# Kernel tuning notes

Measured on AMD Instinct MI355X. Metric: run time of the kernel, lower is better.

Reference implementation:

```python
import jax, jax.numpy as jnp
import numpy as np

NUM_USERS = 100000
NUM_ITEMS = 50000
N_NODES = NUM_USERS + NUM_ITEMS
D = 64
N_LAYERS = 3
E = 2000000
B = 1024
ALPHA_PREF = 1.0


def setup_inputs() -> dict:
    key = jax.random.key(0)
    k1, k2, k3, k4 = jax.random.split(key, 4)
    embed = jax.random.normal(k1, (N_NODES, D), dtype=jnp.float32) * 0.1
    edge_index = jax.random.randint(k2, (2, E), 0, N_NODES, dtype=jnp.int32)
    users = jax.random.randint(k3, (B,), 0, NUM_USERS, dtype=jnp.int32)
    items = jax.random.randint(k4, (B,), 0, NUM_ITEMS, dtype=jnp.int32)
    return {"embed": embed, "edge_index": edge_index, "users": users, "items": items}


def _lightgcn_propagate(x, row, col, norm):
    # message: norm * x[row] (x_j = source), aggregated (add) at col (target)
    msg = norm[:, None] * x[row]                      # [E, D]
    return jnp.zeros_like(x).at[col].add(msg)         # [N, D]


def reference(embed, edge_index, users, items):
    row, col = edge_index[0], edge_index[1]
    n = embed.shape[0]
    # degree normalization (depends only on edge_index; same every layer)
    deg = jnp.zeros((n,), jnp.float32).at[row].add(1.0)
    deg_inv = jnp.clip(deg, 1.0, None) ** -0.5
    norm = deg_inv[row] * deg_inv[col]                # [E]

    x = embed
    for _ in range(N_LAYERS):
        x = _lightgcn_propagate(x, row, col, norm)

    u_emb = x[users]                                  # [B, D]
    i_emb = x[items + NUM_USERS]                      # [B, D]

    # mask = (row == users[:,None]) flattened selection of col; edge e is
    # selected once per batch element b with users[b] == row[e] -> multiplicity
    cnt = jnp.zeros((n,), jnp.float32).at[users].add(1.0)
    mult = cnt[row]                                   # [E] selection multiplicity

    # PreferenceShapley surrogate: softmax over selected neighbor embeddings
    # of alpha_pref * <neigh_emb, mean(u_emb)>, flattened over the batch.
    context = u_emb.mean(0)                           # [D]
    neigh = x[col]                                    # [E, D]
    logits = ALPHA_PREF * (neigh @ context)           # [E]
    masked = jnp.where(mult > 0, logits, -jnp.inf)
    mx = jnp.max(masked)
    ew = mult * jnp.exp(logits - mx)                  # [E] weighted exp (0 where unselected)
    z = jnp.clip(ew.sum(), 1e-12, None)
    neigh_aggr = (ew[:, None] * neigh).sum(0) / z     # [D]

    score = (u_emb * i_emb).sum(-1) + u_emb @ neigh_aggr  # [B]
    return jax.nn.sigmoid(score)
```

## Files before the change

kernel.cpp:

```cpp
#include <hip/hip_runtime.h>
#include <float.h>
#include <math.h>

#define NUM_USERS 100000
#define NUM_ITEMS 50000
#define NNODES    150000
#define DIM       64
#define NEDGE     2000000
#define BATCH     1024
#define SEL_CAP   (1 << 18)
#define LOGIT_BLOCKS 512

#define SLICES   512
#define EPS      3908
#define NBUK     293

__device__ __forceinline__ float wave_sum64(float v) {
    #pragma unroll
    for (int off = 32; off > 0; off >>= 1) v += __shfl_xor(v, off, 64);
    return v;
}

__device__ __forceinline__ float bf2f(unsigned short s) {
    return __uint_as_float(((unsigned int)s) << 16);
}
__device__ __forceinline__ unsigned short f2bf(float f) {
    unsigned int u = __float_as_uint(f);
    return (unsigned short)((u + 0x7fffu + ((u >> 16) & 1u)) >> 16);
}


__global__ __launch_bounds__(512) void bhist_kernel(
        const int* __restrict__ row, const int* __restrict__ col,
        const int* __restrict__ ucnt,
        unsigned short* __restrict__ cntR, unsigned short* __restrict__ cntC,
        unsigned char* __restrict__ rkR, unsigned char* __restrict__ rkC,
        int* __restrict__ n_sel, int* __restrict__ sel_col, float* __restrict__ sel_w) {
    __shared__ unsigned int hr[NBUK], hc[NBUK];
    __shared__ int lcnt, lbase;
    __shared__ int2 buf[256];
    int blk = blockIdx.x, t = threadIdx.x;
    for (int i = t; i < NBUK; i += 512) { hr[i] = 0; hc[i] = 0; }
    if (t == 0) lcnt = 0;
    __syncthreads();
    int e0 = blk * EPS;
    int e1 = e0 + EPS; if (e1 > NEDGE) e1 = NEDGE;
    for (int base = e0 + t * 4; base < e1; base += 2048) {
        if (base + 4 <= e1) {
            int4 r4 = *(const int4*)(row + base);
            int4 c4 = *(const int4*)(col + base);
            uchar4 a, b;
            a.x = (unsigned char)atomicAdd(&hr[r4.x >> 9], 1u);
            a.y = (unsigned char)atomicAdd(&hr[r4.y >> 9], 1u);
            a.z = (unsigned char)atomicAdd(&hr[r4.z >> 9], 1u);
            a.w = (unsigned char)atomicAdd(&hr[r4.w >> 9], 1u);
            b.x = (unsigned char)atomicAdd(&hc[c4.x >> 9], 1u);
            b.y = (unsigned char)atomicAdd(&hc[c4.y >> 9], 1u);
            b.z = (unsigned char)atomicAdd(&hc[c4.z >> 9], 1u);
            b.w = (unsigned char)atomicAdd(&hc[c4.w >> 9], 1u);
            *(uchar4*)(rkR + base) = a;
            *(uchar4*)(rkC + base) = b;
            int u0 = ucnt[r4.x], u1 = ucnt[r4.y], u2 = ucnt[r4.z], u3 = ucnt[r4.w];
            if (u0 > 0) { int i = atomicAdd(&lcnt, 1); if (i < 256) buf[i] = make_int2(c4.x, u0); }
            if (u1 > 0) { int i = atomicAdd(&lcnt, 1); if (i < 256) buf[i] = make_int2(c4.y, u1); }
            if (u2 > 0) { int i = atomicAdd(&lcnt, 1); if (i < 256) buf[i] = make_int2(c4.z, u2); }
            if (u3 > 0) { int i = atomicAdd(&lcnt, 1); if (i < 256) buf[i] = make_int2(c4.w, u3); }
        } else {
            for (int e = base; e < e1; ++e) {
                int r = row[e], c = col[e];
                rkR[e] = (unsigned char)atomicAdd(&hr[r >> 9], 1u);
                rkC[e] = (unsigned char)atomicAdd(&hc[c >> 9], 1u);
                int u = ucnt[r];
                if (u > 0) { int i = atomicAdd(&lcnt, 1); if (i < 256) buf[i] = make_int2(c, u); }
            }
        }
    }
    __syncthreads();
    for (int i = t; i < NBUK; i += 512) {
        cntR[(size_t)blk * NBUK + i] = (unsigned short)hr[i];
        cntC[(size_t)blk * NBUK + i] = (unsigned short)hc[i];
    }
    if (t == 0) {
        int c = lcnt; c = c < 256 ? c : 256;
        lbase = atomicAdd(n_sel, c);
    }
    __syncthreads();
    int c = lcnt; c = c < 256 ? c : 256;
    int b = lbase;
    for (int i = t; i < c; i += 512) {
        int o = b + i;
        if (o < SEL_CAP) { sel_col[o] = buf[i].x; sel_w[o] = (float)buf[i].y; }
    }
}


__global__ __launch_bounds__(512) void bprefix1_kernel(
        const unsigned short* __restrict__ cntR, const unsigned short* __restrict__ cntC,
        unsigned short* __restrict__ offR, unsigned short* __restrict__ offC,
        int* __restrict__ totRC) {
    int side = blockIdx.x / NBUK;
    int b = blockIdx.x - side * NBUK;
    const unsigned short* cnt = side ? cntC : cntR;
    unsigned short* off = side ? offC : offR;
    __shared__ int sm[512];
    int t = threadIdx.x;
    int v = (int)cnt[(size_t)t * NBUK + b];
    sm[t] = v;
    __syncthreads();
    for (int o = 1; o < 512; o <<= 1) {
        int x = (t >= o) ? sm[t - o] : 0;
        __syncthreads();
        sm[t] += x;
        __syncthreads();
    }
    off[(size_t)t * NBUK + b] = (unsigned short)(sm[t] - v);
    if (t == 511) totRC[side * NBUK + b] = sm[511];
}

__global__ __launch_bounds__(512) void bprefix2_kernel(
        const int* __restrict__ totRC, int* __restrict__ baseR, int* __restrict__ baseC) {
    const int* tot = totRC + blockIdx.x * NBUK;
    int* base = blockIdx.x ? baseC : baseR;
    __shared__ int sm[512];
    int t = threadIdx.x;
    int v = (t < NBUK) ? tot[t] : 0;
    sm[t] = v;
    __syncthreads();
    for (int o = 1; o < 512; o <<= 1) {
        int x = (t >= o) ? sm[t - o] : 0;
        __syncthreads();
        sm[t] += x;
        __syncthreads();
    }
    if (t < NBUK) base[t] = sm[t] - v;
    if (t == NBUK - 1) base[NBUK] = sm[t];
}


__global__ __launch_bounds__(512) void place_kernel(
        const int* __restrict__ row, const int* __restrict__ col,
        const unsigned char* __restrict__ rkR, const unsigned char* __restrict__ rkC,
        const unsigned short* __restrict__ cntR, const unsigned short* __restrict__ cntC,
        const unsigned short* __restrict__ offR, const unsigned short* __restrict__ offC,
        const int* __restrict__ baseR, const int* __restrict__ baseC,
        unsigned short* __restrict__ midR, unsigned int* __restrict__ midC) {
    __shared__ int lofC[NBUK], lofR[NBUK], posC[NBUK], posR[NBUK];
    __shared__ int cCl[NBUK], cRl[NBUK];
    __shared__ int scan_tmp[512];
    __shared__ unsigned int   stC[EPS];
    __shared__ unsigned short stR[EPS];
    int blk = blockIdx.x, t = threadIdx.x;
    if (t < NBUK) {
        cCl[t] = (int)cntC[(size_t)blk * NBUK + t];
        cRl[t] = (int)cntR[(size_t)blk * NBUK + t];
        posC[t] = baseC[t] + (int)offC[(size_t)blk * NBUK + t];
        posR[t] = baseR[t] + (int)offR[(size_t)blk * NBUK + t];
    }
    __syncthreads();
    scan_tmp[t] = (t < NBUK) ? cCl[t] : 0;
    __syncthreads();
    for (int o = 1; o < 512; o <<= 1) {
        int v = (t >= o) ? scan_tmp[t - o] : 0;
        __syncthreads();
        scan_tmp[t] += v;
        __syncthreads();
    }
    if (t < NBUK) lofC[t] = scan_tmp[t] - cCl[t];
    __syncthreads();
    scan_tmp[t] = (t < NBUK) ? cRl[t] : 0;
    __syncthreads();
    for (int o = 1; o < 512; o <<= 1) {
        int v = (t >= o) ? scan_tmp[t - o] : 0;
        __syncthreads();
        scan_tmp[t] += v;
        __syncthreads();
    }
    if (t < NBUK) lofR[t] = scan_tmp[t] - cRl[t];
    __syncthreads();
    int e0 = blk * EPS;
    int e1 = e0 + EPS; if (e1 > NEDGE) e1 = NEDGE;
    for (int base = e0 + t * 4; base < e1; base += 2048) {
        if (base + 4 <= e1) {
            int4 r4 = *(const int4*)(row + base);
            int4 c4 = *(const int4*)(col + base);
            uchar4 kr = *(const uchar4*)(rkR + base);
            uchar4 kc = *(const uchar4*)(rkC + base);
            stC[lofC[c4.x >> 9] + (int)kc.x] = ((unsigned int)(c4.x & 511) << 18) | (unsigned int)r4.x;
            stC[lofC[c4.y >> 9] + (int)kc.y] = ((unsigned int)(c4.y & 511) << 18) | (unsigned int)r4.y;
            stC[lofC[c4.z >> 9] + (int)kc.z] = ((unsigned int)(c4.z & 511) << 18) | (unsigned int)r4.z;
            stC[lofC[c4.w >> 9] + (int)kc.w] = ((unsigned int)(c4.w & 511) << 18) | (unsigned int)r4.w;
            stR[lofR[r4.x >> 9] + (int)kr.x] = (unsigned short)(r4.x & 511);
            stR[lofR[r4.y >> 9] + (int)kr.y] = (unsigned short)(r4.y & 511);
            stR[lofR[r4.z >> 9] + (int)kr.z] = (unsigned short)(r4.z & 511);
            stR[lofR[r4.w >> 9] + (int)kr.w] = (unsigned short)(r4.w & 511);
        } else {
            for (int e = base; e < e1; ++e) {
                int r = row[e], c = col[e];
                stC[lofC[c >> 9] + (int)rkC[e]] = ((unsigned int)(c & 511) << 18) | (unsigned int)r;
                stR[lofR[r >> 9] + (int)rkR[e]] = (unsigned short)(r & 511);
            }
        }
    }
    __syncthreads();
    int wave = t >> 6, lane = t & 63;
    for (int b = wave; b < NBUK; b += 8) {
        int n = cCl[b], lo = lofC[b], dst = posC[b];
        for (int i = lane; i < n; i += 64) midC[dst + i] = stC[lo + i];
        n = cRl[b]; lo = lofR[b]; dst = posR[b];
        for (int i = lane; i < n; i += 64) midR[dst + i] = stR[lo + i];
    }
}


__global__ __launch_bounds__(1024) void bfinal_kernel(
        const unsigned int* __restrict__ midC, const int* __restrict__ baseC,
        const unsigned short* __restrict__ midR, const int* __restrict__ baseR,
        const float4* __restrict__ embed,
        int* __restrict__ rptr, int* __restrict__ src_sorted,
        float* __restrict__ dinv, float* __restrict__ dinv2,
        uint2* __restrict__ y0) {
    __shared__ int cnt[512], sm[512], cur[512];
    __shared__ float dinvL[512];
    int b = blockIdx.x, t = threadIdx.x;
    int s0 = baseC[b], s1 = baseC[b + 1];
    if (t < 512) cnt[t] = 0;
    __syncthreads();
    for (int i = s0 + t; i < s1; i += 1024) atomicAdd(&cnt[midC[i] >> 18], 1);
    __syncthreads();
    if (t < 512) sm[t] = cnt[t];
    __syncthreads();
    for (int off = 1; off < 512; off <<= 1) {
        int v = 0;
        if (t < 512 && t >= off) v = sm[t - off];
        __syncthreads();
        if (t < 512) sm[t] += v;
        __syncthreads();
    }
    if (t < 512) {
        int excl = s0 + sm[t] - cnt[t];
        int n = b * 512 + t;
        if (n < NNODES) rptr[n] = excl;
        cur[t] = excl;
    }
    if (b == NBUK - 1 && t == 0) rptr[NNODES] = s1;
    if (b == 0 && t < 16) y0[(size_t)NNODES * 16 + t] = make_uint2(0u, 0u);
    __syncthreads();
    for (int i = s0 + t; i < s1; i += 1024) {
        unsigned int v = midC[i];
        int dst = atomicAdd(&cur[v >> 18], 1);
        src_sorted[dst] = (int)(v & 0x3FFFFu);
    }
    __syncthreads();
    if (t < 512) cnt[t] = 0;
    __syncthreads();
    int r0 = baseR[b], r1 = baseR[b + 1];
    for (int i = r0 + t; i < r1; i += 1024) atomicAdd(&cnt[midR[i]], 1);
    __syncthreads();
    if (t < 512) {
        int n = b * 512 + t;
        if (n < NNODES) {
            float d = fmaxf((float)cnt[t], 1.0f);
            float di = rsqrtf(d);
            dinv[n] = di; dinv2[n] = 1.0f / d;
            dinvL[t] = di;
        }
    }
    __syncthreads();
    int nbase = b * 512;
    int nmax = NNODES - nbase; if (nmax > 512) nmax = 512;
    if (nmax < 0) nmax = 0;
    for (int i = t; i < nmax * 16; i += 1024) {
        int ln = i >> 4, slot = i & 15;
        float d = dinvL[ln];
        float4 v = embed[(size_t)(nbase + ln) * 16 + slot];
        unsigned int w0 = (unsigned int)f2bf(v.x * d) | ((unsigned int)f2bf(v.y * d) << 16);
        unsigned int w1 = (unsigned int)f2bf(v.z * d) | ((unsigned int)f2bf(v.w * d) << 16);
        y0[(size_t)(nbase + ln) * 16 + slot] = make_uint2(w0, w1);
    }
}


#define ACC8(V) do { \
    a0 += __uint_as_float((V).x << 16); a1 += __uint_as_float((V).x & 0xffff0000u); \
    a2 += __uint_as_float((V).y << 16); a3 += __uint_as_float((V).y & 0xffff0000u); \
    a4 += __uint_as_float((V).z << 16); a5 += __uint_as_float((V).z & 0xffff0000u); \
    a6 += __uint_as_float((V).w << 16); a7 += __uint_as_float((V).w & 0xffff0000u); \
} while (0)

__global__ __launch_bounds__(256, 8) void prop_kernel(
        const uint4* __restrict__ x_in, uint4* __restrict__ x_out,
        const int* __restrict__ ptr, const int* __restrict__ src,
        const float* __restrict__ scale) {
    int gid  = blockIdx.x * blockDim.x + threadIdx.x;
    int node = gid >> 3;
    int sl   = gid & 7;
    if (node > NNODES) return;
    if (node == NNODES) {
        x_out[(size_t)node * 8 + sl] = make_uint4(0u, 0u, 0u, 0u);
        return;
    }
    int i = ptr[node], e = ptr[node + 1];
    float sc = scale[node];
    float a0 = 0.f, a1 = 0.f, a2 = 0.f, a3 = 0.f;
    float a4 = 0.f, a5 = 0.f, a6 = 0.f, a7 = 0.f;
    int p0, p1, p2, p3;
    if (i + 4 <= e) { p0 = src[i]; p1 = src[i + 1]; p2 = src[i + 2]; p3 = src[i + 3]; }
    while (i + 8 <= e) {
        uint4 w0 = x_in[p0 * 8 + sl];
        uint4 w1 = x_in[p1 * 8 + sl];
        uint4 w2 = x_in[p2 * 8 + sl];
        uint4 w3 = x_in[p3 * 8 + sl];
        p0 = src[i + 4]; p1 = src[i + 5]; p2 = src[i + 6]; p3 = src[i + 7];
        i += 4;
        ACC8(w0); ACC8(w1); ACC8(w2); ACC8(w3);
    }
    if (i + 4 <= e) {
        uint4 w0 = x_in[p0 * 8 + sl];
        uint4 w1 = x_in[p1 * 8 + sl];
        uint4 w2 = x_in[p2 * 8 + sl];
        uint4 w3 = x_in[p3 * 8 + sl];
        i += 4;
        ACC8(w0); ACC8(w1); ACC8(w2); ACC8(w3);
    }
    if (i < e) {
        int q0 = src[i];
        int q1 = (i + 1 < e) ? src[i + 1] : NNODES;
        int q2 = (i + 2 < e) ? src[i + 2] : NNODES;
        uint4 w0 = x_in[q0 * 8 + sl];
        uint4 w1 = x_in[q1 * 8 + sl];
        uint4 w2 = x_in[q2 * 8 + sl];
        ACC8(w0); ACC8(w1); ACC8(w2);
    }
    uint4 o;
    o.x = (unsigned int)f2bf(a0 * sc) | ((unsigned int)f2bf(a1 * sc) << 16);
    o.y = (unsigned int)f2bf(a2 * sc) | ((unsigned int)f2bf(a3 * sc) << 16);
    o.z = (unsigned int)f2bf(a4 * sc) | ((unsigned int)f2bf(a5 * sc) << 16);
    o.w = (unsigned int)f2bf(a6 * sc) | ((unsigned int)f2bf(a7 * sc) << 16);
    x_out[(size_t)node * 8 + sl] = o;
}


__global__ void ucnt_kernel(const int* __restrict__ users, int* __restrict__ ucnt) {
    int b = blockIdx.x * blockDim.x + threadIdx.x;
    if (b < BATCH) atomicAdd(&ucnt[users[b]], 1);
}

__global__ __launch_bounds__(256) void ctx_part_kernel(
        const unsigned short* __restrict__ x, const int* __restrict__ users,
        float* __restrict__ partial) {
    __shared__ float sm[256];
    int lane = threadIdx.x & 63, wl = threadIdx.x >> 6;
    int b = blockIdx.x * 4 + wl;
    float v = (b < BATCH) ? bf2f(x[users[b] * DIM + lane]) : 0.0f;
    sm[threadIdx.x] = v;
    __syncthreads();
    if (wl == 0)
        partial[blockIdx.x * 64 + lane] =
            sm[lane] + sm[64 + lane] + sm[128 + lane] + sm[192 + lane];
}

__global__ __launch_bounds__(256) void ctx_reduce_kernel(
        const float* __restrict__ partial, float* __restrict__ ctx) {
    __shared__ float sm[256];
    int lane = threadIdx.x & 63, wl = threadIdx.x >> 6;
    float acc = 0.0f;
    for (int i = wl; i < 256; i += 4) acc += partial[i * 64 + lane];
    sm[threadIdx.x] = acc;
    __syncthreads();
    if (wl == 0)
        ctx[lane] = (sm[lane] + sm[64 + lane] + sm[128 + lane] + sm[192 + lane])
                    * (1.0f / BATCH);
}

__global__ void softmax_kernel(const unsigned short* __restrict__ x,
                               const float* __restrict__ ctx,
                               const int* __restrict__ sel_col,
                               const float* __restrict__ sel_w,
                               const int* __restrict__ n_sel_p,
                               float* __restrict__ S, float* __restrict__ zp) {
    __shared__ float smS[4 * 64];
    __shared__ float smZ[4];
    int lane = threadIdx.x & 63, wl = threadIdx.x >> 6;
    int n = *n_sel_p; if (n > SEL_CAP) n = SEL_CAP;
    float c = ctx[lane];
    float accS = 0.0f, accZ = 0.0f;
    int stride = gridDim.x * 4;
    for (int idx = blockIdx.x * 4 + wl; idx < n; idx += stride) {
        int node = sel_col[idx];
        float xv = bf2f(x[node * DIM + lane]);
        float v = wave_sum64(xv * c);
        float w = sel_w[idx] * __expf(v);
        accS = fmaf(w, xv, accS);
        accZ += w;
    }
    smS[wl * 64 + lane] = accS;
    if (lane == 0) smZ[wl] = accZ;
    __syncthreads();
    if (wl == 0) {
        float s = smS[lane] + smS[64 + lane] + smS[128 + lane] + smS[192 + lane];
        atomicAdd(&S[lane], s);
    }
    if (threadIdx.x == 0) atomicAdd(zp, smZ[0] + smZ[1] + smZ[2] + smZ[3]);
}

__global__ void score_kernel(const unsigned short* __restrict__ x, const int* __restrict__ users,
                             const int* __restrict__ items, const float* __restrict__ S,
                             const float* __restrict__ zp, float* __restrict__ out) {
    int gid = blockIdx.x * blockDim.x + threadIdx.x;
    int b = gid >> 6, lane = gid & 63;
    if (b >= BATCH) return;
    float z = fmaxf(*zp, 1e-12f);
    float na = S[lane] / z;
    int u = users[b], it = items[b] + NUM_USERS;
    float v = bf2f(x[u * DIM + lane]) * (bf2f(x[it * DIM + lane]) + na);
    v = wave_sum64(v);
    if (lane == 0) out[b] = 1.0f / (1.0f + __expf(-v));
}


extern "C" void kernel_launch(void* const* d_in, const int* in_sizes, int n_in,
                              void* d_out, int out_size, void* d_ws, size_t ws_size,
                              hipStream_t stream) {
    const float* embed = (const float*)d_in[0];
    const int*   edge  = (const int*)d_in[1];
    const int*   row   = edge;
    const int*   col   = edge + NEDGE;
    const int*   users = (const int*)d_in[2];
    const int*   items = (const int*)d_in[3];
    float*       out   = (float*)d_out;
    char*        ws    = (char*)d_ws;

    size_t off = 0;
    auto A = [&](size_t bytes) { size_t o = off; off += (bytes + 255) & ~(size_t)255; return o; };
    size_t o_mid   = A((size_t)NEDGE * 4 + (size_t)NEDGE * 2);
    size_t o_xa    = A((size_t)(NNODES + 1) * DIM * 2);
    size_t o_xb    = A((size_t)(NNODES + 1) * DIM * 2);
    size_t o_src   = A((size_t)NEDGE * 4);
    size_t o_rkR   = A((size_t)SLICES * EPS);
    size_t o_rkC   = A((size_t)SLICES * EPS);
    size_t o_cntR  = A((size_t)SLICES * NBUK * 2);
    size_t o_cntC  = A((size_t)SLICES * NBUK * 2);
    size_t o_offR  = A((size_t)SLICES * NBUK * 2);
    size_t o_offC  = A((size_t)SLICES * NBUK * 2);
    size_t o_tot   = A((size_t)2 * NBUK * 4);
    size_t o_baseR = A((size_t)(NBUK + 1) * 4);
    size_t o_baseC = A((size_t)(NBUK + 1) * 4);
    size_t o_selc  = A((size_t)SEL_CAP * 4);
    size_t o_selw  = A((size_t)SEL_CAP * 4);
    size_t o_part  = A((size_t)256 * 64 * 4);
    size_t o_zero  = off;
    size_t o_ucnt  = A((size_t)NNODES * 4);
    size_t o_misc  = A(1024);
    size_t zero_bytes = off - o_zero;
    size_t o_dinv  = A((size_t)NNODES * 4);
    size_t o_dinv2 = A((size_t)NNODES * 4);
    size_t o_rptr  = A((size_t)(NNODES + 1) * 4);
    size_t o_ctx   = A(256);

    unsigned int*   midC = (unsigned int*)(ws + o_mid);
    unsigned short* midR = (unsigned short*)(ws + o_mid + (size_t)NEDGE * 4);
    unsigned short* xa   = (unsigned short*)(ws + o_xa);
    unsigned short* xb   = (unsigned short*)(ws + o_xb);
    int*   srcS  = (int*)(ws + o_src);
    unsigned char* rkR = (unsigned char*)(ws + o_rkR);
    unsigned char* rkC = (unsigned char*)(ws + o_rkC);
    unsigned short* cntR = (unsigned short*)(ws + o_cntR);
    unsigned short* cntC = (unsigned short*)(ws + o_cntC);
    unsigned short* offR = (unsigned short*)(ws + o_offR);
    unsigned short* offC = (unsigned short*)(ws + o_offC);
    int*   totRC = (int*)(ws + o_tot);
    int*   baseR = (int*)(ws + o_baseR);
    int*   baseC = (int*)(ws + o_baseC);
    int*   selc  = (int*)(ws + o_selc);
    float* selw  = (float*)(ws + o_selw);
    float* part  = (float*)(ws + o_part);
    int*   ucnt  = (int*)(ws + o_ucnt);
    int*   nsel  = (int*)(ws + o_misc);
    float* zp    = (float*)(ws + o_misc + 8);
    float* S     = (float*)(ws + o_misc + 256);
    float* dinv  = (float*)(ws + o_dinv);
    float* dinv2 = (float*)(ws + o_dinv2);
    int*   rptr  = (int*)(ws + o_rptr);
    float* ctx   = (float*)(ws + o_ctx);

    hipMemsetAsync(ws + o_zero, 0, zero_bytes, stream);

    ucnt_kernel<<<(BATCH + 255) / 256, 256, 0, stream>>>(users, ucnt);

    bhist_kernel<<<SLICES, 512, 0, stream>>>(row, col, ucnt, cntR, cntC, rkR, rkC,
                                             nsel, selc, selw);
    bprefix1_kernel<<<2 * NBUK, 512, 0, stream>>>(cntR, cntC, offR, offC, totRC);
    bprefix2_kernel<<<2, 512, 0, stream>>>(totRC, baseR, baseC);
    place_kernel<<<SLICES, 512, 0, stream>>>(row, col, rkR, rkC, cntR, cntC,
                                             offR, offC, baseR, baseC, midR, midC);
    bfinal_kernel<<<NBUK, 1024, 0, stream>>>(midC, baseC, midR, baseR,
                                             (const float4*)embed, rptr, srcS,
                                             dinv, dinv2, (uint2*)xa);

    int prop_blocks = ((NNODES + 1) * 8 + 255) / 256;
    prop_kernel<<<prop_blocks, 256, 0, stream>>>((const uint4*)xa, (uint4*)xb, rptr, srcS, dinv2);
    prop_kernel<<<prop_blocks, 256, 0, stream>>>((const uint4*)xb, (uint4*)xa, rptr, srcS, dinv2);
    prop_kernel<<<prop_blocks, 256, 0, stream>>>((const uint4*)xa, (uint4*)xb, rptr, srcS, dinv);

    ctx_part_kernel<<<256, 256, 0, stream>>>(xb, users, part);
    ctx_reduce_kernel<<<1, 256, 0, stream>>>(part, ctx);
    softmax_kernel<<<LOGIT_BLOCKS, 256, 0, stream>>>(xb, ctx, selc, selw, nsel, S, zp);

    score_kernel<<<(BATCH * 64 + 255) / 256, 256, 0, stream>>>(xb, users, items, S, zp, out);
}
```

Before: 304.9 us.

## Compute final propagation layer only for nodes consumed downstream

The third propagation layer now computes output rows only for batch users, batch items, and the selected neighbor columns, instead of all nodes. Only those rows are read by the context, softmax and score kernels, so the full-graph final pass is mostly wasted gather work. The list kernel launches a grid sized for the selection cap and exits threads past the actual count. Duplicate entries in the list get recomputed redundantly.

```diff
diff --git a/kernel.cpp b/kernel.cpp
--- a/kernel.cpp
+++ b/kernel.cpp
@@ -287,18 +287,10 @@
     a6 += __uint_as_float((V).w << 16); a7 += __uint_as_float((V).w & 0xffff0000u); \
 } while (0)
 
-__global__ __launch_bounds__(256, 8) void prop_kernel(
+__device__ __forceinline__ void prop_node(
         const uint4* __restrict__ x_in, uint4* __restrict__ x_out,
         const int* __restrict__ ptr, const int* __restrict__ src,
-        const float* __restrict__ scale) {
-    int gid  = blockIdx.x * blockDim.x + threadIdx.x;
-    int node = gid >> 3;
-    int sl   = gid & 7;
-    if (node > NNODES) return;
-    if (node == NNODES) {
-        x_out[(size_t)node * 8 + sl] = make_uint4(0u, 0u, 0u, 0u);
-        return;
-    }
+        const float* __restrict__ scale, int node, int sl) {
     int i = ptr[node], e = ptr[node + 1];
     float sc = scale[node];
     float a0 = 0.f, a1 = 0.f, a2 = 0.f, a3 = 0.f;
@@ -337,6 +329,44 @@
     o.z = (unsigned int)f2bf(a4 * sc) | ((unsigned int)f2bf(a5 * sc) << 16);
     o.w = (unsigned int)f2bf(a6 * sc) | ((unsigned int)f2bf(a7 * sc) << 16);
     x_out[(size_t)node * 8 + sl] = o;
+}
+
+__global__ __launch_bounds__(256, 8) void prop_kernel(
+        const uint4* __restrict__ x_in, uint4* __restrict__ x_out,
+        const int* __restrict__ ptr, const int* __restrict__ src,
+        const float* __restrict__ scale) {
+    int gid  = blockIdx.x * blockDim.x + threadIdx.x;
+    int node = gid >> 3;
+    int sl   = gid & 7;
+    if (node > NNODES) return;
+    if (node == NNODES) {
+        x_out[(size_t)node * 8 + sl] = make_uint4(0u, 0u, 0u, 0u);
+        return;
+    }
+    prop_node(x_in, x_out, ptr, src, scale, node, sl);
+}
+
+__global__ __launch_bounds__(256, 8) void prop_list_kernel(
+        const uint4* __restrict__ x_in, uint4* __restrict__ x_out,
+        const int* __restrict__ ptr, const int* __restrict__ src,
+        const float* __restrict__ scale,
+        const int* __restrict__ users, const int* __restrict__ items,
+        const int* __restrict__ sel_col, const int* __restrict__ n_sel_p) {
+    int gid = blockIdx.x * blockDim.x + threadIdx.x;
+    int li  = gid >> 3;
+    int sl  = gid & 7;
+    int node;
+    if (li < BATCH) {
+        node = users[li];
+    } else if (li < 2 * BATCH) {
+        node = items[li - BATCH] + NUM_USERS;
+    } else {
+        int j = li - 2 * BATCH;
+        int n = *n_sel_p; if (n > SEL_CAP) n = SEL_CAP;
+        if (j >= n) return;
+        node = sel_col[j];
+    }
+    prop_node(x_in, x_out, ptr, src, scale, node, sl);
 }
 
 
@@ -500,7 +530,10 @@
     int prop_blocks = ((NNODES + 1) * 8 + 255) / 256;
     prop_kernel<<<prop_blocks, 256, 0, stream>>>((const uint4*)xa, (uint4*)xb, rptr, srcS, dinv2);
     prop_kernel<<<prop_blocks, 256, 0, stream>>>((const uint4*)xb, (uint4*)xa, rptr, srcS, dinv2);
-    prop_kernel<<<prop_blocks, 256, 0, stream>>>((const uint4*)xa, (uint4*)xb, rptr, srcS, dinv);
+    int list_blocks = ((2 * BATCH + SEL_CAP) * 8 + 255) / 256;
+    prop_list_kernel<<<list_blocks, 256, 0, stream>>>((const uint4*)xa, (uint4*)xb,
+                                                      rptr, srcS, dinv,
+                                                      users, items, selc, nsel);
 
     ctx_part_kernel<<<256, 256, 0, stream>>>(xb, users, part);
     ctx_reduce_kernel<<<1, 256, 0, stream>>>(part, ctx);
```

Measured after the change: 277.4 us. -9.0%, faster.
